# Kernel tuning notes

Hardware: AMD Instinct MI355X
Metric: run time of the kernel (lower is better)

## Reference

```python
import jax, jax.numpy as jnp
import numpy as np


def setup_inputs() -> dict:
    key = jax.random.key(0)
    k1, k2, k3, k4 = jax.random.split(key, 4)
    B, A, C = 16, 65536, 21  # batch, anchors, num_classes+1 (20 fg classes + background)
    loc_preds = jax.random.normal(k1, (B, A, 4), dtype=jnp.float32)
    loc_targets = jax.random.normal(k2, (B, A, 4), dtype=jnp.float32)
    cls_preds = jax.random.normal(k3, (B, A, C), dtype=jnp.float32)
    # -1 = ignore, 0 = background/negative, 1..20 = positive classes
    cls_targets = jax.random.randint(k4, (B, A), -1, C)
    pos = cls_targets > 0
    return {
        "loc_preds": loc_preds,
        "loc_targets": loc_targets,
        "cls_preds": cls_preds,
        "cls_targets": cls_targets,
        "pos": pos,
        "verbose": 0,
    }


def reference(loc_preds, loc_targets, cls_preds, cls_targets, pos, verbose):
    eps = 1e-7
    num_pos = jnp.sum(pos).astype(loc_preds.dtype)

    # smooth L1 over positive anchors (sum reduction, beta=1), mask instead of gather
    posf = pos[..., None].astype(loc_preds.dtype)          # [B, A, 1]
    d = loc_preds - loc_targets
    ad = jnp.abs(d)
    sl1 = jnp.where(ad < 1.0, 0.5 * d * d, ad - 0.5)
    loc_loss = jnp.sum(sl1 * posf)

    # focal loss over non-ignored anchors (cls_targets > -1)
    pos_neg = (cls_targets > -1)[..., None].astype(cls_preds.dtype)  # [B, A, 1]
    C = cls_preds.shape[-1]
    y = jax.nn.one_hot(cls_targets, C, dtype=cls_preds.dtype)  # -1 -> all zeros
    p = jax.nn.softmax(cls_preds, axis=-1)
    p = jnp.clip(p, eps, 1.0 - eps)
    fl = -y * jnp.log(p) * (1.0 - p) ** 2
    cls_loss = jnp.sum(fl * pos_neg)

    return (loc_loss + cls_loss) / num_pos
```

## Files before the change

### kernel.cpp

```cpp
#include <hip/hip_runtime.h>

#define NCLS 21
#define BLK 256

__device__ __forceinline__ float4 load_f4_unaligned(const float* p) {
    float4 v;
    __builtin_memcpy(&v, p, 16);
    return v;
}

__global__ __launch_bounds__(BLK) void focal_main(
    const float* __restrict__ loc_p,
    const float* __restrict__ loc_t,
    const float* __restrict__ cls_p,
    const int*   __restrict__ cls_t,
    float2* __restrict__ partials,
    int n_anchors)
{
    const int tid  = threadIdx.x;
    const int wave = tid >> 6;
    const int lane = tid & 63;
    const long long a = (long long)blockIdx.x * BLK + tid;

    float acc  = 0.0f;
    float npos = 0.0f;

    if (a < n_anchors) {
        const int t = cls_t[a];
        const float4 lp = ((const float4*)loc_p)[a];
        const float4 lt = ((const float4*)loc_t)[a];

        const float* g = cls_p + a * NCLS;
        float row[NCLS];
        #pragma unroll
        for (int k = 0; k < 5; ++k) {
            float4 r = load_f4_unaligned(g + k * 4);
            row[k * 4 + 0] = r.x; row[k * 4 + 1] = r.y;
            row[k * 4 + 2] = r.z; row[k * 4 + 3] = r.w;
        }
        row[20] = g[20];

        {
            float d0 = lp.x - lt.x, d1 = lp.y - lt.y, d2 = lp.z - lt.z, d3 = lp.w - lt.w;
            float a0 = fabsf(d0), a1 = fabsf(d1), a2 = fabsf(d2), a3 = fabsf(d3);
            float s = 0.0f;
            s += (a0 < 1.0f) ? 0.5f * d0 * d0 : a0 - 0.5f;
            s += (a1 < 1.0f) ? 0.5f * d1 * d1 : a1 - 0.5f;
            s += (a2 < 1.0f) ? 0.5f * d2 * d2 : a2 - 0.5f;
            s += (a3 < 1.0f) ? 0.5f * d3 * d3 : a3 - 0.5f;
            if (t > 0) { acc = s; npos = 1.0f; }
        }

        if (t >= 0) {
            float m = row[0];
            #pragma unroll
            for (int j = 1; j < NCLS; ++j) m = fmaxf(m, row[j]);
            float s = 0.0f;
            #pragma unroll
            for (int j = 0; j < NCLS; ++j) s += __expf(row[j] - m);
            float pt = __expf(row[t] - m) / s;
            pt = fminf(fmaxf(pt, 1e-7f), 1.0f - 1e-7f);
            float om = 1.0f - pt;
            acc += -__logf(pt) * om * om;
        }
    }

    #pragma unroll
    for (int off = 32; off > 0; off >>= 1) {
        acc  += __shfl_down(acc,  off, 64);
        npos += __shfl_down(npos, off, 64);
    }
    if (lane == 0)
        partials[blockIdx.x * 4 + wave] = make_float2(acc, npos);
}

#define RBLK 1024
__global__ __launch_bounds__(RBLK) void focal_reduce(
    const float2* __restrict__ partials, float* __restrict__ out, int npart)
{
    __shared__ float red[32];
    float L = 0.0f, P = 0.0f;
    for (int i = threadIdx.x; i < npart; i += RBLK) {
        float2 v = partials[i];
        L += v.x; P += v.y;
    }
    #pragma unroll
    for (int off = 32; off > 0; off >>= 1) {
        L += __shfl_down(L, off, 64);
        P += __shfl_down(P, off, 64);
    }
    const int wave = threadIdx.x >> 6, lane = threadIdx.x & 63;
    if (lane == 0) { red[wave * 2] = L; red[wave * 2 + 1] = P; }
    __syncthreads();
    if (threadIdx.x == 0) {
        float Ls = 0.0f, Ps = 0.0f;
        #pragma unroll
        for (int w = 0; w < RBLK / 64; ++w) { Ls += red[w * 2]; Ps += red[w * 2 + 1]; }
        out[0] = Ls / Ps;
    }
}

extern "C" void kernel_launch(void* const* d_in, const int* in_sizes, int n_in,
                              void* d_out, int out_size, void* d_ws, size_t ws_size,
                              hipStream_t stream)
{
    const float* loc_p = (const float*)d_in[0];
    const float* loc_t = (const float*)d_in[1];
    const float* cls_p = (const float*)d_in[2];
    const int*   cls_t = (const int*)d_in[3];
    float*  out = (float*)d_out;
    float2* ws  = (float2*)d_ws;

    const int n_anchors = in_sizes[3];
    const int blocks = (n_anchors + BLK - 1) / BLK;

    focal_main<<<blocks, BLK, 0, stream>>>(loc_p, loc_t, cls_p, cls_t, ws, n_anchors);
    focal_reduce<<<1, RBLK, 0, stream>>>(ws, out, blocks * 4);
}
```

Measured before the change: 170.5 us.

## Fuse final reduction into main kernel via last-block atomic counter, two anchors per thread

The separate reduce kernel is removed. Each block now writes its partial sums and increments a global atomic counter, and the last block to finish performs the final reduction. Each thread also processes two anchors so that more loads are in flight, and the grid has half as many blocks. A memset of the counter is added before each launch, and keeping two 21-float rows per thread raises register pressure.

```diff
diff --git a/kernel.cpp b/kernel.cpp
--- a/kernel.cpp
+++ b/kernel.cpp
@@ -2,101 +2,132 @@
 
 #define NCLS 21
 #define BLK 256
+#define APT 2
+#define SPAN (BLK * APT)
 
-__device__ __forceinline__ float4 load_f4_unaligned(const float* p) {
+__device__ __forceinline__ float4 load_f4u(const float* p) {
     float4 v;
     __builtin_memcpy(&v, p, 16);
     return v;
 }
 
-__global__ __launch_bounds__(BLK) void focal_main(
+__device__ __forceinline__ void smooth_l1(int t, const float4& lp, const float4& lt,
+                                          float& acc, float& npos) {
+    float d0 = lp.x - lt.x, d1 = lp.y - lt.y, d2 = lp.z - lt.z, d3 = lp.w - lt.w;
+    float a0 = fabsf(d0), a1 = fabsf(d1), a2 = fabsf(d2), a3 = fabsf(d3);
+    float s = 0.0f;
+    s += (a0 < 1.0f) ? 0.5f * d0 * d0 : a0 - 0.5f;
+    s += (a1 < 1.0f) ? 0.5f * d1 * d1 : a1 - 0.5f;
+    s += (a2 < 1.0f) ? 0.5f * d2 * d2 : a2 - 0.5f;
+    s += (a3 < 1.0f) ? 0.5f * d3 * d3 : a3 - 0.5f;
+    if (t > 0) { acc += s; npos += 1.0f; }
+}
+
+__device__ __forceinline__ void focal_term(int t, const float* row, float& acc) {
+    if (t >= 0) {
+        float m = row[0];
+        #pragma unroll
+        for (int j = 1; j < NCLS; ++j) m = fmaxf(m, row[j]);
+        float s = 0.0f;
+        #pragma unroll
+        for (int j = 0; j < NCLS; ++j) s += __expf(row[j] - m);
+        float pt = __expf(row[t] - m) / s;
+        pt = fminf(fmaxf(pt, 1e-7f), 1.0f - 1e-7f);
+        float om = 1.0f - pt;
+        acc += -__logf(pt) * om * om;
+    }
+}
+
+__global__ __launch_bounds__(BLK) void focal_fused(
     const float* __restrict__ loc_p,
     const float* __restrict__ loc_t,
     const float* __restrict__ cls_p,
     const int*   __restrict__ cls_t,
-    float2* __restrict__ partials,
-    int n_anchors)
+    unsigned int* __restrict__ counter,
+    float*        __restrict__ pf,
+    float*        __restrict__ out,
+    int n_anchors, int nblocks)
 {
+    __shared__ float redL[4], redP[4];
+    __shared__ int last_flag;
+
     const int tid  = threadIdx.x;
     const int wave = tid >> 6;
     const int lane = tid & 63;
-    const long long a = (long long)blockIdx.x * BLK + tid;
+    const long long a0 = (long long)blockIdx.x * SPAN + tid;
+    const long long a1 = a0 + BLK;
 
-    float acc  = 0.0f;
-    float npos = 0.0f;
+    float acc = 0.0f, npos = 0.0f;
 
-    if (a < n_anchors) {
-        const int t = cls_t[a];
-        const float4 lp = ((const float4*)loc_p)[a];
-        const float4 lt = ((const float4*)loc_t)[a];
-
-        const float* g = cls_p + a * NCLS;
-        float row[NCLS];
+    int t0 = -1, t1 = -1;
+    float4 lp0, lt0, lp1, lt1;
+    float r0[NCLS], r1[NCLS];
+    const bool v0 = (a0 < n_anchors), v1 = (a1 < n_anchors);
+    if (v0) {
+        t0  = cls_t[a0];
+        lp0 = ((const float4*)loc_p)[a0];
+        lt0 = ((const float4*)loc_t)[a0];
+        const float* g = cls_p + a0 * NCLS;
         #pragma unroll
         for (int k = 0; k < 5; ++k) {
-            float4 r = load_f4_unaligned(g + k * 4);
-            row[k * 4 + 0] = r.x; row[k * 4 + 1] = r.y;
-            row[k * 4 + 2] = r.z; row[k * 4 + 3] = r.w;
+            float4 r = load_f4u(g + k * 4);
+            r0[k*4+0] = r.x; r0[k*4+1] = r.y; r0[k*4+2] = r.z; r0[k*4+3] = r.w;
         }
-        row[20] = g[20];
+        r0[20] = g[20];
+    }
+    if (v1) {
+        t1  = cls_t[a1];
+        lp1 = ((const float4*)loc_p)[a1];
+        lt1 = ((const float4*)loc_t)[a1];
+        const float* g = cls_p + a1 * NCLS;
+        #pragma unroll
+        for (int k = 0; k < 5; ++k) {
+            float4 r = load_f4u(g + k * 4);
+            r1[k*4+0] = r.x; r1[k*4+1] = r.y; r1[k*4+2] = r.z; r1[k*4+3] = r.w;
+        }
+        r1[20] = g[20];
+    }
 
-        {
-            float d0 = lp.x - lt.x, d1 = lp.y - lt.y, d2 = lp.z - lt.z, d3 = lp.w - lt.w;
-            float a0 = fabsf(d0), a1 = fabsf(d1), a2 = fabsf(d2), a3 = fabsf(d3);
-            float s = 0.0f;
-            s += (a0 < 1.0f) ? 0.5f * d0 * d0 : a0 - 0.5f;
-            s += (a1 < 1.0f) ? 0.5f * d1 * d1 : a1 - 0.5f;
-            s += (a2 < 1.0f) ? 0.5f * d2 * d2 : a2 - 0.5f;
-            s += (a3 < 1.0f) ? 0.5f * d3 * d3 : a3 - 0.5f;
-            if (t > 0) { acc = s; npos = 1.0f; }
-        }
-
-        if (t >= 0) {
-            float m = row[0];
-            #pragma unroll
-            for (int j = 1; j < NCLS; ++j) m = fmaxf(m, row[j]);
-            float s = 0.0f;
-            #pragma unroll
-            for (int j = 0; j < NCLS; ++j) s += __expf(row[j] - m);
-            float pt = __expf(row[t] - m) / s;
-            pt = fminf(fmaxf(pt, 1e-7f), 1.0f - 1e-7f);
-            float om = 1.0f - pt;
-            acc += -__logf(pt) * om * om;
-        }
-    }
+    if (v0) { smooth_l1(t0, lp0, lt0, acc, npos); focal_term(t0, r0, acc); }
+    if (v1) { smooth_l1(t1, lp1, lt1, acc, npos); focal_term(t1, r1, acc); }
 
     #pragma unroll
     for (int off = 32; off > 0; off >>= 1) {
         acc  += __shfl_down(acc,  off, 64);
         npos += __shfl_down(npos, off, 64);
     }
-    if (lane == 0)
-        partials[blockIdx.x * 4 + wave] = make_float2(acc, npos);
-}
+    if (lane == 0) { redL[wave] = acc; redP[wave] = npos; }
+    __syncthreads();
 
-#define RBLK 1024
-__global__ __launch_bounds__(RBLK) void focal_reduce(
-    const float2* __restrict__ partials, float* __restrict__ out, int npart)
-{
-    __shared__ float red[32];
-    float L = 0.0f, P = 0.0f;
-    for (int i = threadIdx.x; i < npart; i += RBLK) {
-        float2 v = partials[i];
-        L += v.x; P += v.y;
+    if (tid == 0) {
+        float L = redL[0] + redL[1] + redL[2] + redL[3];
+        float P = redP[0] + redP[1] + redP[2] + redP[3];
+        __hip_atomic_store(&pf[2 * blockIdx.x],     L, __ATOMIC_RELAXED, __HIP_MEMORY_SCOPE_AGENT);
+        __hip_atomic_store(&pf[2 * blockIdx.x + 1], P, __ATOMIC_RELAXED, __HIP_MEMORY_SCOPE_AGENT);
+        unsigned int old = __hip_atomic_fetch_add(counter, 1u, __ATOMIC_ACQ_REL,
+                                                  __HIP_MEMORY_SCOPE_AGENT);
+        last_flag = (old == (unsigned int)(nblocks - 1));
     }
-    #pragma unroll
-    for (int off = 32; off > 0; off >>= 1) {
-        L += __shfl_down(L, off, 64);
-        P += __shfl_down(P, off, 64);
-    }
-    const int wave = threadIdx.x >> 6, lane = threadIdx.x & 63;
-    if (lane == 0) { red[wave * 2] = L; red[wave * 2 + 1] = P; }
     __syncthreads();
-    if (threadIdx.x == 0) {
-        float Ls = 0.0f, Ps = 0.0f;
+
+    if (last_flag) {
+        float L = 0.0f, P = 0.0f;
+        for (int i = tid; i < nblocks; i += BLK) {
+            L += __hip_atomic_load(&pf[2 * i],     __ATOMIC_RELAXED, __HIP_MEMORY_SCOPE_AGENT);
+            P += __hip_atomic_load(&pf[2 * i + 1], __ATOMIC_RELAXED, __HIP_MEMORY_SCOPE_AGENT);
+        }
         #pragma unroll
-        for (int w = 0; w < RBLK / 64; ++w) { Ls += red[w * 2]; Ps += red[w * 2 + 1]; }
-        out[0] = Ls / Ps;
+        for (int off = 32; off > 0; off >>= 1) {
+            L += __shfl_down(L, off, 64);
+            P += __shfl_down(P, off, 64);
+        }
+        if (lane == 0) { redL[wave] = L; redP[wave] = P; }
+        __syncthreads();
+        if (tid == 0) {
+            float Ls = redL[0] + redL[1] + redL[2] + redL[3];
+            float Ps = redP[0] + redP[1] + redP[2] + redP[3];
+            out[0] = Ls / Ps;
+        }
     }
 }
 
@@ -108,12 +139,15 @@
     const float* loc_t = (const float*)d_in[1];
     const float* cls_p = (const float*)d_in[2];
     const int*   cls_t = (const int*)d_in[3];
-    float*  out = (float*)d_out;
-    float2* ws  = (float2*)d_ws;
+    float* out = (float*)d_out;
+
+    unsigned int* counter = (unsigned int*)d_ws;
+    float* pf = (float*)((char*)d_ws + 16);
 
     const int n_anchors = in_sizes[3];
-    const int blocks = (n_anchors + BLK - 1) / BLK;
+    const int blocks = (n_anchors + SPAN - 1) / SPAN;
 
-    focal_main<<<blocks, BLK, 0, stream>>>(loc_p, loc_t, cls_p, cls_t, ws, n_anchors);
-    focal_reduce<<<1, RBLK, 0, stream>>>(ws, out, blocks * 4);
+    hipMemsetAsync(d_ws, 0, 16, stream);
+    focal_fused<<<blocks, BLK, 0, stream>>>(loc_p, loc_t, cls_p, cls_t,
+                                            counter, pf, out, n_anchors, blocks);
 }
```

After: 265.7 us. 55.8% more time.

## Process two anchors per thread and reduce partials per block

Applied to the files above, without the earlier changes.

Each thread now loads and processes two anchors, with all loads issued before compute so more memory requests are in flight per thread. The softmax target exponent is picked out with a select inside the sum loop instead of a dynamically indexed register array, which avoids local-memory spills. Per-wave partials are combined in shared memory so each block writes one partial, which shrinks the final reduce. The cost is higher register pressure and half as many blocks.

```diff
diff --git a/kernel.cpp b/kernel.cpp
--- a/kernel.cpp
+++ b/kernel.cpp
@@ -2,11 +2,53 @@
 
 #define NCLS 21
 #define BLK 256
+#define APT 2
+#define SPAN (BLK * APT)
 
-__device__ __forceinline__ float4 load_f4_unaligned(const float* p) {
+__device__ __forceinline__ float4 load_f4u(const float* p) {
     float4 v;
     __builtin_memcpy(&v, p, 16);
     return v;
+}
+
+__device__ __forceinline__ float fmax4(const float4& v) {
+    return fmaxf(fmaxf(v.x, v.y), fmaxf(v.z, v.w));
+}
+__device__ __forceinline__ float4 fmax44(const float4& a, const float4& b) {
+    return make_float4(fmaxf(a.x, b.x), fmaxf(a.y, b.y),
+                       fmaxf(a.z, b.z), fmaxf(a.w, b.w));
+}
+
+__device__ __forceinline__ float focal_regs(
+    int t, const float4& c0, const float4& c1, const float4& c2,
+    const float4& c3, const float4& c4, float c20)
+{
+    float m = fmaxf(fmax4(fmax44(fmax44(c0, c1), fmax44(c2, c3))),
+                    fmaxf(fmax4(c4), c20));
+    float s = 0.0f, et = 0.0f;
+#define FSTEP(val, idx) { float e = __expf((val) - m); s += e; et = (t == (idx)) ? e : et; }
+    FSTEP(c0.x, 0)  FSTEP(c0.y, 1)  FSTEP(c0.z, 2)  FSTEP(c0.w, 3)
+    FSTEP(c1.x, 4)  FSTEP(c1.y, 5)  FSTEP(c1.z, 6)  FSTEP(c1.w, 7)
+    FSTEP(c2.x, 8)  FSTEP(c2.y, 9)  FSTEP(c2.z, 10) FSTEP(c2.w, 11)
+    FSTEP(c3.x, 12) FSTEP(c3.y, 13) FSTEP(c3.z, 14) FSTEP(c3.w, 15)
+    FSTEP(c4.x, 16) FSTEP(c4.y, 17) FSTEP(c4.z, 18) FSTEP(c4.w, 19)
+    FSTEP(c20,  20)
+#undef FSTEP
+    float pt = et / s;
+    pt = fminf(fmaxf(pt, 1e-7f), 1.0f - 1e-7f);
+    float om = 1.0f - pt;
+    return -__logf(pt) * om * om;
+}
+
+__device__ __forceinline__ float smooth_l1(const float4& lp, const float4& lt) {
+    float d0 = lp.x - lt.x, d1 = lp.y - lt.y, d2 = lp.z - lt.z, d3 = lp.w - lt.w;
+    float a0 = fabsf(d0), a1 = fabsf(d1), a2 = fabsf(d2), a3 = fabsf(d3);
+    float s = 0.0f;
+    s += (a0 < 1.0f) ? 0.5f * d0 * d0 : a0 - 0.5f;
+    s += (a1 < 1.0f) ? 0.5f * d1 * d1 : a1 - 0.5f;
+    s += (a2 < 1.0f) ? 0.5f * d2 * d2 : a2 - 0.5f;
+    s += (a3 < 1.0f) ? 0.5f * d3 * d3 : a3 - 0.5f;
+    return s;
 }
 
 __global__ __launch_bounds__(BLK) void focal_main(
@@ -17,52 +59,46 @@
     float2* __restrict__ partials,
     int n_anchors)
 {
+    __shared__ float redL[4], redP[4];
+
     const int tid  = threadIdx.x;
     const int wave = tid >> 6;
     const int lane = tid & 63;
-    const long long a = (long long)blockIdx.x * BLK + tid;
+    const long long a0 = (long long)blockIdx.x * SPAN + tid;
+    const long long a1 = a0 + BLK;
 
-    float acc  = 0.0f;
-    float npos = 0.0f;
+    float acc = 0.0f, npos = 0.0f;
+    const bool v0 = (a0 < n_anchors), v1 = (a1 < n_anchors);
 
-    if (a < n_anchors) {
-        const int t = cls_t[a];
-        const float4 lp = ((const float4*)loc_p)[a];
-        const float4 lt = ((const float4*)loc_t)[a];
+    int t0 = -1, t1 = -1;
+    float4 lp0, lt0, lp1, lt1;
+    float4 c00, c01, c02, c03, c04; float c0_20 = 0.0f;
+    float4 c10, c11, c12, c13, c14; float c1_20 = 0.0f;
 
-        const float* g = cls_p + a * NCLS;
-        float row[NCLS];
-        #pragma unroll
-        for (int k = 0; k < 5; ++k) {
-            float4 r = load_f4_unaligned(g + k * 4);
-            row[k * 4 + 0] = r.x; row[k * 4 + 1] = r.y;
-            row[k * 4 + 2] = r.z; row[k * 4 + 3] = r.w;
-        }
-        row[20] = g[20];
+    if (v0) {
+        t0  = cls_t[a0];
+        lp0 = ((const float4*)loc_p)[a0];
+        lt0 = ((const float4*)loc_t)[a0];
+        const float* g = cls_p + a0 * NCLS;
+        c00 = load_f4u(g);      c01 = load_f4u(g + 4);  c02 = load_f4u(g + 8);
+        c03 = load_f4u(g + 12); c04 = load_f4u(g + 16); c0_20 = g[20];
+    }
+    if (v1) {
+        t1  = cls_t[a1];
+        lp1 = ((const float4*)loc_p)[a1];
+        lt1 = ((const float4*)loc_t)[a1];
+        const float* g = cls_p + a1 * NCLS;
+        c10 = load_f4u(g);      c11 = load_f4u(g + 4);  c12 = load_f4u(g + 8);
+        c13 = load_f4u(g + 12); c14 = load_f4u(g + 16); c1_20 = g[20];
+    }
 
-        {
-            float d0 = lp.x - lt.x, d1 = lp.y - lt.y, d2 = lp.z - lt.z, d3 = lp.w - lt.w;
-            float a0 = fabsf(d0), a1 = fabsf(d1), a2 = fabsf(d2), a3 = fabsf(d3);
-            float s = 0.0f;
-            s += (a0 < 1.0f) ? 0.5f * d0 * d0 : a0 - 0.5f;
-            s += (a1 < 1.0f) ? 0.5f * d1 * d1 : a1 - 0.5f;
-            s += (a2 < 1.0f) ? 0.5f * d2 * d2 : a2 - 0.5f;
-            s += (a3 < 1.0f) ? 0.5f * d3 * d3 : a3 - 0.5f;
-            if (t > 0) { acc = s; npos = 1.0f; }
-        }
-
-        if (t >= 0) {
-            float m = row[0];
-            #pragma unroll
-            for (int j = 1; j < NCLS; ++j) m = fmaxf(m, row[j]);
-            float s = 0.0f;
-            #pragma unroll
-            for (int j = 0; j < NCLS; ++j) s += __expf(row[j] - m);
-            float pt = __expf(row[t] - m) / s;
-            pt = fminf(fmaxf(pt, 1e-7f), 1.0f - 1e-7f);
-            float om = 1.0f - pt;
-            acc += -__logf(pt) * om * om;
-        }
+    if (v0) {
+        if (t0 > 0)  { acc += smooth_l1(lp0, lt0); npos += 1.0f; }
+        if (t0 >= 0) acc += focal_regs(t0, c00, c01, c02, c03, c04, c0_20);
+    }
+    if (v1) {
+        if (t1 > 0)  { acc += smooth_l1(lp1, lt1); npos += 1.0f; }
+        if (t1 >= 0) acc += focal_regs(t1, c10, c11, c12, c13, c14, c1_20);
     }
 
     #pragma unroll
@@ -70,8 +106,11 @@
         acc  += __shfl_down(acc,  off, 64);
         npos += __shfl_down(npos, off, 64);
     }
-    if (lane == 0)
-        partials[blockIdx.x * 4 + wave] = make_float2(acc, npos);
+    if (lane == 0) { redL[wave] = acc; redP[wave] = npos; }
+    __syncthreads();
+    if (tid == 0)
+        partials[blockIdx.x] = make_float2(redL[0] + redL[1] + redL[2] + redL[3],
+                                           redP[0] + redP[1] + redP[2] + redP[3]);
 }
 
 #define RBLK 1024
@@ -112,8 +151,8 @@
     float2* ws  = (float2*)d_ws;
 
     const int n_anchors = in_sizes[3];
-    const int blocks = (n_anchors + BLK - 1) / BLK;
+    const int blocks = (n_anchors + SPAN - 1) / SPAN;
 
     focal_main<<<blocks, BLK, 0, stream>>>(loc_p, loc_t, cls_p, cls_t, ws, n_anchors);
-    focal_reduce<<<1, RBLK, 0, stream>>>(ws, out, blocks * 4);
+    focal_reduce<<<1, RBLK, 0, stream>>>(ws, out, blocks);
 }
```

Measured after the change: 166.8 us. -2.2%, faster.

## Use fixed grid with register-prefetched anchors and select-based target extraction

Applied to the files above, without the earlier changes.

The kernel now launches a fixed 1024-block grid where each thread handles K=4 strided anchors. It loads the next anchor into registers while computing the current one, to hide global memory latency. The target-class exponential is picked with a per-element select instead of dynamically indexing a local array, which avoids a possible scratch-memory spill. Per-wave partials are combined through shared memory so only one partial per block goes to the final reduce. The trade-off is that coverage is hardcoded to GRID*BLK*K anchors, so inputs larger than that would be silently truncated.

```diff
diff --git a/kernel.cpp b/kernel.cpp
--- a/kernel.cpp
+++ b/kernel.cpp
@@ -2,11 +2,73 @@
 
 #define NCLS 21
 #define BLK 256
+#define GRID 1024
+#define K 4
 
-__device__ __forceinline__ float4 load_f4_unaligned(const float* p) {
-    float4 v;
-    __builtin_memcpy(&v, p, 16);
-    return v;
+__device__ __forceinline__ float4 load_f4u(const float* p) {
+    float4 v; __builtin_memcpy(&v, p, 16); return v;
+}
+
+__device__ __forceinline__ float fmax4(const float4& v) {
+    return fmaxf(fmaxf(v.x, v.y), fmaxf(v.z, v.w));
+}
+__device__ __forceinline__ float4 fmax44(const float4& a, const float4& b) {
+    return make_float4(fmaxf(a.x, b.x), fmaxf(a.y, b.y),
+                       fmaxf(a.z, b.z), fmaxf(a.w, b.w));
+}
+
+struct Anchor {
+    int t;
+    float4 lp, lt;
+    float4 c0, c1, c2, c3, c4;
+    float c20;
+};
+
+__device__ __forceinline__ void load_anchor(
+    const float* __restrict__ loc_p, const float* __restrict__ loc_t,
+    const float* __restrict__ cls_p, const int* __restrict__ cls_t,
+    long long a, int n_anchors, Anchor& d)
+{
+    d.t = -1;
+    if (a < n_anchors) {
+        d.t  = cls_t[a];
+        d.lp = ((const float4*)loc_p)[a];
+        d.lt = ((const float4*)loc_t)[a];
+        const float* g = cls_p + a * NCLS;
+        d.c0 = load_f4u(g);      d.c1 = load_f4u(g + 4);
+        d.c2 = load_f4u(g + 8);  d.c3 = load_f4u(g + 12);
+        d.c4 = load_f4u(g + 16); d.c20 = g[20];
+    }
+}
+
+__device__ __forceinline__ void process(const Anchor& d, float& acc, float& npos) {
+    if (d.t > 0) {
+        float d0 = d.lp.x - d.lt.x, d1 = d.lp.y - d.lt.y;
+        float d2 = d.lp.z - d.lt.z, d3 = d.lp.w - d.lt.w;
+        float a0 = fabsf(d0), a1 = fabsf(d1), a2 = fabsf(d2), a3 = fabsf(d3);
+        acc += (a0 < 1.0f) ? 0.5f * d0 * d0 : a0 - 0.5f;
+        acc += (a1 < 1.0f) ? 0.5f * d1 * d1 : a1 - 0.5f;
+        acc += (a2 < 1.0f) ? 0.5f * d2 * d2 : a2 - 0.5f;
+        acc += (a3 < 1.0f) ? 0.5f * d3 * d3 : a3 - 0.5f;
+        npos += 1.0f;
+    }
+    if (d.t >= 0) {
+        float m = fmaxf(fmax4(fmax44(fmax44(d.c0, d.c1), fmax44(d.c2, d.c3))),
+                        fmaxf(fmax4(d.c4), d.c20));
+        float s = 0.0f, et = 0.0f;
+#define FSTEP(val, idx) { float e = __expf((val) - m); s += e; et = (d.t == (idx)) ? e : et; }
+        FSTEP(d.c0.x, 0)  FSTEP(d.c0.y, 1)  FSTEP(d.c0.z, 2)  FSTEP(d.c0.w, 3)
+        FSTEP(d.c1.x, 4)  FSTEP(d.c1.y, 5)  FSTEP(d.c1.z, 6)  FSTEP(d.c1.w, 7)
+        FSTEP(d.c2.x, 8)  FSTEP(d.c2.y, 9)  FSTEP(d.c2.z, 10) FSTEP(d.c2.w, 11)
+        FSTEP(d.c3.x, 12) FSTEP(d.c3.y, 13) FSTEP(d.c3.z, 14) FSTEP(d.c3.w, 15)
+        FSTEP(d.c4.x, 16) FSTEP(d.c4.y, 17) FSTEP(d.c4.z, 18) FSTEP(d.c4.w, 19)
+        FSTEP(d.c20,  20)
+#undef FSTEP
+        float pt = et / s;
+        pt = fminf(fmaxf(pt, 1e-7f), 1.0f - 1e-7f);
+        float om = 1.0f - pt;
+        acc += -__logf(pt) * om * om;
+    }
 }
 
 __global__ __launch_bounds__(BLK) void focal_main(
@@ -17,52 +79,26 @@
     float2* __restrict__ partials,
     int n_anchors)
 {
+    __shared__ float redL[4], redP[4];
+
     const int tid  = threadIdx.x;
     const int wave = tid >> 6;
     const int lane = tid & 63;
-    const long long a = (long long)blockIdx.x * BLK + tid;
+    const long long stride = (long long)GRID * BLK;
+    long long a = (long long)blockIdx.x * BLK + tid;
 
-    float acc  = 0.0f;
-    float npos = 0.0f;
+    float acc = 0.0f, npos = 0.0f;
 
-    if (a < n_anchors) {
-        const int t = cls_t[a];
-        const float4 lp = ((const float4*)loc_p)[a];
-        const float4 lt = ((const float4*)loc_t)[a];
-
-        const float* g = cls_p + a * NCLS;
-        float row[NCLS];
-        #pragma unroll
-        for (int k = 0; k < 5; ++k) {
-            float4 r = load_f4_unaligned(g + k * 4);
-            row[k * 4 + 0] = r.x; row[k * 4 + 1] = r.y;
-            row[k * 4 + 2] = r.z; row[k * 4 + 3] = r.w;
-        }
-        row[20] = g[20];
-
-        {
-            float d0 = lp.x - lt.x, d1 = lp.y - lt.y, d2 = lp.z - lt.z, d3 = lp.w - lt.w;
-            float a0 = fabsf(d0), a1 = fabsf(d1), a2 = fabsf(d2), a3 = fabsf(d3);
-            float s = 0.0f;
-            s += (a0 < 1.0f) ? 0.5f * d0 * d0 : a0 - 0.5f;
-            s += (a1 < 1.0f) ? 0.5f * d1 * d1 : a1 - 0.5f;
-            s += (a2 < 1.0f) ? 0.5f * d2 * d2 : a2 - 0.5f;
-            s += (a3 < 1.0f) ? 0.5f * d3 * d3 : a3 - 0.5f;
-            if (t > 0) { acc = s; npos = 1.0f; }
-        }
-
-        if (t >= 0) {
-            float m = row[0];
-            #pragma unroll
-            for (int j = 1; j < NCLS; ++j) m = fmaxf(m, row[j]);
-            float s = 0.0f;
-            #pragma unroll
-            for (int j = 0; j < NCLS; ++j) s += __expf(row[j] - m);
-            float pt = __expf(row[t] - m) / s;
-            pt = fminf(fmaxf(pt, 1e-7f), 1.0f - 1e-7f);
-            float om = 1.0f - pt;
-            acc += -__logf(pt) * om * om;
-        }
+    Anchor cur, nxt;
+    load_anchor(loc_p, loc_t, cls_p, cls_t, a, n_anchors, cur);
+    #pragma unroll
+    for (int i = 0; i < K; ++i) {
+        const long long an = a + stride;
+        if (i + 1 < K)
+            load_anchor(loc_p, loc_t, cls_p, cls_t, an, n_anchors, nxt);
+        process(cur, acc, npos);
+        cur = nxt;
+        a = an;
     }
 
     #pragma unroll
@@ -70,8 +106,11 @@
         acc  += __shfl_down(acc,  off, 64);
         npos += __shfl_down(npos, off, 64);
     }
-    if (lane == 0)
-        partials[blockIdx.x * 4 + wave] = make_float2(acc, npos);
+    if (lane == 0) { redL[wave] = acc; redP[wave] = npos; }
+    __syncthreads();
+    if (tid == 0)
+        partials[blockIdx.x] = make_float2(redL[0] + redL[1] + redL[2] + redL[3],
+                                           redP[0] + redP[1] + redP[2] + redP[3]);
 }
 
 #define RBLK 1024
@@ -112,8 +151,7 @@
     float2* ws  = (float2*)d_ws;
 
     const int n_anchors = in_sizes[3];
-    const int blocks = (n_anchors + BLK - 1) / BLK;
 
-    focal_main<<<blocks, BLK, 0, stream>>>(loc_p, loc_t, cls_p, cls_t, ws, n_anchors);
-    focal_reduce<<<1, RBLK, 0, stream>>>(ws, out, blocks * 4);
+    focal_main<<<GRID, BLK, 0, stream>>>(loc_p, loc_t, cls_p, cls_t, ws, n_anchors);
+    focal_reduce<<<1, RBLK, 0, stream>>>(ws, out, GRID);
 }
```

Measured after the change: 169.7 us. No clear change (-0.5%).
